# Optimization experiments

Hardware: AMD Instinct MI355X
Metric: run time of the kernel (lower is better)

Reference implementation:

```python
import jax, jax.numpy as jnp
import numpy as np

NODES = 81
NODE_DIM = 2
IN_DIM = NODES * NODE_DIM  # 162
D = 256
H = 16
HD = D // H
DFF = 2048
T, B, E = 1024, 8, 648


def _layernorm(x, w, b, eps=1e-5):
    m = x.mean(-1, keepdims=True)
    v = x.var(-1, keepdims=True)
    return (x - m) / jnp.sqrt(v + eps) * w + b


def setup_inputs() -> dict:
    key = jax.random.key(0)
    ks = jax.random.split(key, 12)
    s = 0.02
    W = lambda k, shape: jax.random.normal(k, shape, jnp.float32) * s
    return {
        "src": jax.random.normal(ks[0], (T, B, IN_DIM), jnp.float32),
        "edge_index": jax.random.randint(ks[1], (2, E), 0, NODES),
        "gcn_w": W(ks[2], (NODE_DIM, NODE_DIM)),
        "gcn_b": jnp.zeros((NODE_DIM,), jnp.float32),
        "fc_w": W(ks[3], (IN_DIM, D)),
        "fc_b": jnp.zeros((D,), jnp.float32),
        "wq": W(ks[4], (D, D)), "bq": jnp.zeros((D,), jnp.float32),
        "wk": W(ks[5], (D, D)), "bk": jnp.zeros((D,), jnp.float32),
        "wv": W(ks[6], (D, D)), "bv": jnp.zeros((D,), jnp.float32),
        "wo": W(ks[7], (D, D)), "bo": jnp.zeros((D,), jnp.float32),
        "ln1_w": jnp.ones((D,), jnp.float32), "ln1_b": jnp.zeros((D,), jnp.float32),
        "ffn_w1": W(ks[8], (D, DFF)), "ffn_b1": jnp.zeros((DFF,), jnp.float32),
        "ffn_w2": W(ks[9], (DFF, D)), "ffn_b2": jnp.zeros((D,), jnp.float32),
        "ln2_w": jnp.ones((D,), jnp.float32), "ln2_b": jnp.zeros((D,), jnp.float32),
        "dec_w": W(ks[10], (D, IN_DIM)), "dec_b": jnp.zeros((IN_DIM,), jnp.float32),
    }


def reference(src, edge_index, gcn_w, gcn_b, fc_w, fc_b, wq, bq, wk, bk, wv, bv,
              wo, bo, ln1_w, ln1_b, ffn_w1, ffn_b1, ffn_w2, ffn_b2, ln2_w, ln2_b,
              dec_w, dec_b):
    t, b, _ = src.shape
    # ---- batched GCNConv(2,2): all T*B tiny graphs share one adjacency ----
    # src[t,b] = [in_flow(81), out_flow(81)] -> node features [81, 2]
    xg = jnp.swapaxes(src.reshape(t, b, NODE_DIM, NODES), -1, -2)  # [T,B,81,2]
    row, col = edge_index[0], edge_index[1]
    A = jnp.zeros((NODES, NODES), src.dtype).at[col, row].add(1.0)
    A = A + jnp.eye(NODES, dtype=src.dtype)          # add self-loops
    deg = A.sum(1)
    dinv = jnp.where(deg > 0, 1.0 / jnp.sqrt(deg), 0.0)
    A_hat = dinv[:, None] * A * dinv[None, :]        # D^-1/2 (A+I) D^-1/2
    hg = jnp.einsum('ij,tbjc->tbic', A_hat, xg @ gcn_w) + gcn_b  # [T,B,81,2]
    # gcn_output.transpose(0,1).view(-1): channel-major flatten
    src2 = jnp.swapaxes(hg, -1, -2).reshape(t, b, IN_DIM)
    # ---- fc + positional encoding ----
    x = src2 @ fc_w + fc_b  # [T,B,D]
    pos = jnp.arange(t, dtype=jnp.float32)[:, None]
    div = jnp.exp(jnp.arange(0, D, 2, dtype=jnp.float32) * (-np.log(10000.0) / D))
    pe = jnp.zeros((t, D), x.dtype).at[:, 0::2].set(jnp.sin(pos * div))
    pe = pe.at[:, 1::2].set(jnp.cos(pos * div))
    x = x + pe[:, None, :]
    # ---- TransformerEncoderLayer (post-norm, relu, causal mask, eval) ----
    q = (x @ wq + bq).reshape(t, b, H, HD)
    k = (x @ wk + bk).reshape(t, b, H, HD)
    v = (x @ wv + bv).reshape(t, b, H, HD)
    scores = jnp.einsum('tbhd,sbhd->bhts', q, k) / jnp.sqrt(jnp.asarray(HD, x.dtype))
    causal = jnp.tril(jnp.ones((t, t), bool))
    scores = jnp.where(causal, scores, jnp.finfo(x.dtype).min)
    attn = jax.nn.softmax(scores, axis=-1)
    ctx = jnp.einsum('bhts,sbhd->tbhd', attn, v).reshape(t, b, D) @ wo + bo
    x = _layernorm(x + ctx, ln1_w, ln1_b)
    ff = jax.nn.relu(x @ ffn_w1 + ffn_b1) @ ffn_w2 + ffn_b2
    x = _layernorm(x + ff, ln2_w, ln2_b)
    return x @ dec_w + dec_b  # [T,B,162]
```

## Files before the change

kernel.cpp:

```cpp
#include <hip/hip_runtime.h>
#include <math.h>

#define T_    1024
#define B_    8
#define D_    256
#define H_    16
#define HD_   16
#define DFF_  2048
#define NODES_ 81
#define INDIM_ 162
#define E_    648
#define M_    (T_*B_)

typedef __bf16 bf16x8 __attribute__((ext_vector_type(8)));
typedef float  f32x4  __attribute__((ext_vector_type(4)));
typedef unsigned short ushort_t;
typedef unsigned int   uint_t;

union bfpack { bf16x8 v; uint_t u[4]; };

__device__ __forceinline__ ushort_t f2bf(float f) {
    union { float f; uint_t u; } c; c.f = f;
    uint_t u = c.u;
    uint_t r = u + 0x7fffu + ((u >> 16) & 1u);
    return (ushort_t)(r >> 16);
}

__device__ __forceinline__ uint_t fbits(float f) {
    union { float f; uint_t u; } c; c.f = f;
    return c.u;
}

__device__ __forceinline__ bf16x8 zero8() {
    bf16x8 v;
#pragma unroll
    for (int e = 0; e < 8; e++) v[e] = (__bf16)0.0f;
    return v;
}

__device__ __forceinline__ void gload_lds16(const void* g, void* l) {
    __builtin_amdgcn_global_load_lds(
        (const __attribute__((address_space(1))) void*)g,
        (__attribute__((address_space(3))) void*)l, 16, 0, 0);
}

__device__ __forceinline__ void trans_tile(
        const float* __restrict__ in, ushort_t* __restrict__ out,
        float (*tile)[33], int K, int N, int Kp, int bx, int by) {
    int k0 = bx * 32, n0 = by * 32;
    int tx = threadIdx.x & 31, ty = threadIdx.x >> 5;
#pragma unroll
    for (int i = 0; i < 4; i++) {
        int r = k0 + ty + i * 8, c = n0 + tx;
        tile[ty + i * 8][tx] = (r < K && c < N) ? in[(size_t)r * N + c] : 0.f;
    }
    __syncthreads();
#pragma unroll
    for (int i = 0; i < 4; i++) {
        int r = n0 + ty + i * 8, c = k0 + tx;
        out[(size_t)r * Kp + c] = f2bf(tile[tx][ty + i * 8]);
    }
}

__global__ __launch_bounds__(256) void prep_all(
        const int* __restrict__ edge, const float* __restrict__ gcn_w,
        const float* __restrict__ gcn_b, const float* __restrict__ fc_w,
        const float* __restrict__ fc_b, const float* __restrict__ src,
        const float* __restrict__ wq, const float* __restrict__ wk,
        const float* __restrict__ wv, const float* __restrict__ wo,
        const float* __restrict__ dec_w, const float* __restrict__ w1,
        const float* __restrict__ w2,
        const float* __restrict__ bq, const float* __restrict__ bk,
        const float* __restrict__ bv,
        ushort_t* __restrict__ weffT, float* __restrict__ beff,
        ushort_t* __restrict__ srcb,
        ushort_t* __restrict__ wqkvT, ushort_t* __restrict__ woT,
        ushort_t* __restrict__ dwT, ushort_t* __restrict__ w1T,
        ushort_t* __restrict__ w2T, float* __restrict__ qkvbias) {
    __shared__ float A[NODES_ * NODES_];
    __shared__ float dinv[NODES_];
    __shared__ float tile[32][33];
    int bid = blockIdx.x;
    int tid = threadIdx.x;
    if (bid < 82) {
        for (int i = tid; i < NODES_ * NODES_; i += 256) A[i] = 0.f;
        __syncthreads();
        for (int e = tid; e < E_; e += 256) {
            int r = edge[e];
            int c = edge[E_ + e];
            atomicAdd(&A[c * NODES_ + r], 1.0f);
        }
        __syncthreads();
        if (tid < NODES_) A[tid * NODES_ + tid] += 1.0f;
        __syncthreads();
        if (tid < NODES_) {
            float s = 0.f;
            for (int k = 0; k < NODES_; k++) s += A[tid * NODES_ + k];
            dinv[tid] = (s > 0.f) ? rsqrtf(s) : 0.f;
        }
        __syncthreads();
        int d = tid, j = bid;
        if (j < NODES_) {
            float s0 = 0.f, s1 = 0.f;
            for (int i = 0; i < NODES_; i++) {
                float a = dinv[i] * A[i * NODES_ + j] * dinv[j];
                s0 += a * fc_w[(0 * NODES_ + i) * D_ + d];
                s1 += a * fc_w[(1 * NODES_ + i) * D_ + d];
            }
            weffT[d * 192 + j]          = f2bf(gcn_w[0] * s0 + gcn_w[1] * s1);
            weffT[d * 192 + NODES_ + j] = f2bf(gcn_w[2] * s0 + gcn_w[3] * s1);
        } else {
            float t0 = 0.f, t1 = 0.f;
            for (int i = 0; i < NODES_; i++) {
                t0 += fc_w[(0 * NODES_ + i) * D_ + d];
                t1 += fc_w[(1 * NODES_ + i) * D_ + d];
            }
            beff[d] = fc_b[d] + gcn_b[0] * t0 + gcn_b[1] * t1;
            for (int c = INDIM_; c < 192; c++) weffT[d * 192 + c] = 0;
        }
    } else if (bid < 1426) {
        int l = bid - 82;
        if (l < 64)        trans_tile(wq,    wqkvT,          tile, D_,   D_,     D_,   l & 7,  l >> 3);
        else if (l < 128)  trans_tile(wk,    wqkvT + 65536,  tile, D_,   D_,     D_,   (l-64) & 7,  (l-64) >> 3);
        else if (l < 192)  trans_tile(wv,    wqkvT + 131072, tile, D_,   D_,     D_,   (l-128) & 7, (l-128) >> 3);
        else if (l < 256)  trans_tile(wo,    woT,            tile, D_,   D_,     D_,   (l-192) & 7, (l-192) >> 3);
        else if (l < 320)  trans_tile(dec_w, dwT,            tile, D_,   INDIM_, D_,   (l-256) & 7, (l-256) >> 3);
        else if (l < 832)  trans_tile(w1,    w1T,            tile, D_,   DFF_,   D_,   (l-320) & 7, (l-320) >> 3);
        else               trans_tile(w2,    w2T,            tile, DFF_, D_,     DFF_, (l-832) & 63, (l-832) >> 6);
    } else if (bid == 1426) {
#pragma unroll
        for (int k = 0; k < 3; k++) {
            int i = k * 256 + tid;
            qkvbias[i] = (i < 256) ? bq[i] : ((i < 512) ? bk[i - 256] : bv[i - 512]);
        }
    } else {
        int r = bid - 1427;
        if (tid < 192)
            srcb[(size_t)r * 192 + tid] =
                (tid < INDIM_) ? f2bf(src[(size_t)r * INDIM_ + tid]) : (ushort_t)0;
    }
}

enum { EP_PE = 0, EP_QKV = 1, EP_PLAIN = 2, EP_RELU = 3, EP_DEC = 4, EP_PART = 5 };

template <int EPI, int TM, int KS>
__global__ __launch_bounds__(256) void gemm_bf16(
        const ushort_t* __restrict__ A, const ushort_t* __restrict__ BT,
        const float* __restrict__ bias, float* __restrict__ Cf,
        ushort_t* __restrict__ Cb, int M, int N, int K) {
    __shared__ ushort_t sA[TM * 64];
    __shared__ ushort_t sB[128 * 64];
    int tid = threadIdx.x;
    int w = tid >> 6, lane = tid & 63;
    int cc = lane & 15, q = lane >> 4;
    int bm = blockIdx.y * TM, bn = blockIdx.x * 128;
    int part = (KS > 1) ? blockIdx.z : 0;
    int kbeg = part * (K / KS), kend = kbeg + K / KS;

    int srow = (lane >> 3);
    int sslot = lane & 7;

    const int NJ = (TM == 128) ? 4 : 2;
    int mbase = (TM == 128) ? ((w >> 1) * 64) : 0;
    int nbase = (TM == 128) ? ((w & 1) * 64) : (w * 32);

    f32x4 acc[4][NJ];
#pragma unroll
    for (int i = 0; i < 4; i++)
#pragma unroll
        for (int j = 0; j < NJ; j++)
#pragma unroll
            for (int e = 0; e < 4; e++) acc[i][j][e] = 0.f;

    for (int k0 = kbeg; k0 < kend; k0 += 64) {
        if (TM == 128) {
#pragma unroll
            for (int i = 0; i < 4; i++) {
                int r = w * 32 + i * 8 + srow;
                const ushort_t* ga = A + (size_t)(bm + r) * K + k0 + ((sslot ^ (r & 7)) * 8);
                gload_lds16(ga, &sA[(w * 32 + i * 8) * 64]);
            }
        } else {
#pragma unroll
            for (int i = 0; i < 2; i++) {
                int r = w * 16 + i * 8 + srow;
                const ushort_t* ga = A + (size_t)(bm + r) * K + k0 + ((sslot ^ (r & 7)) * 8);
                gload_lds16(ga, &sA[(w * 16 + i * 8) * 64]);
            }
        }
#pragma unroll
        for (int i = 0; i < 4; i++) {
            int r = w * 32 + i * 8 + srow;
            const ushort_t* gb = BT + (size_t)(bn + r) * K + k0 + ((sslot ^ (r & 7)) * 8);
            gload_lds16(gb, &sB[(w * 32 + i * 8) * 64]);
        }
        __syncthreads();
#pragma unroll
        for (int ks = 0; ks < 2; ks++) {
            bf16x8 af[4], bfr[NJ];
#pragma unroll
            for (int i = 0; i < 4; i++) {
                int m = mbase + i * 16 + cc;
                int off = m * 64 + (((ks * 4 + q) ^ (cc & 7)) * 8);
                af[i] = *(const bf16x8*)&sA[off];
            }
#pragma unroll
            for (int j = 0; j < NJ; j++) {
                int n = nbase + j * 16 + cc;
                int off = n * 64 + (((ks * 4 + q) ^ (cc & 7)) * 8);
                bfr[j] = *(const bf16x8*)&sB[off];
            }
#pragma unroll
            for (int i = 0; i < 4; i++)
#pragma unroll
                for (int j = 0; j < NJ; j++)
                    acc[i][j] = __builtin_amdgcn_mfma_f32_16x16x32_bf16(af[i], bfr[j], acc[i][j], 0, 0, 0);
        }
        __syncthreads();
    }

#pragma unroll
    for (int i = 0; i < 4; i++) {
#pragma unroll
        for (int j = 0; j < NJ; j++) {
            int col = bn + nbase + j * 16 + cc;
            float bv = 0.f;
            if (EPI == EP_DEC) bv = (col < INDIM_) ? bias[col] : 0.f;
            else if (EPI != EP_PART) bv = bias[col];
#pragma unroll
            for (int reg = 0; reg < 4; reg++) {
                int row = bm + mbase + i * 16 + q * 4 + reg;
                float v = acc[i][j][reg] + bv;
                if (EPI == EP_PE) {
                    int t = row >> 3;
                    float freq = __expf((float)(col & ~1) * (-9.210340371976184f / 256.f));
                    float ang = (float)t * freq;
                    v += (col & 1) ? __cosf(ang) : __sinf(ang);
                    Cf[(size_t)row * N + col] = v;
                    Cb[(size_t)row * N + col] = f2bf(v);
                } else if (EPI == EP_QKV) {
                    int t = row >> 3, b = row & 7;
                    int nn = col & 255, which = col >> 8;
                    int h = nn >> 4, hd = nn & 15;
                    float vq = (which == 0) ? v * 0.25f : v;
                    Cb[(size_t)which * 2097152 +
                       ((size_t)((b * H_ + h) * T_ + t)) * HD_ + hd] = f2bf(vq);
                } else if (EPI == EP_PLAIN) {
                    Cf[(size_t)row * N + col] = v;
                } else if (EPI == EP_RELU) {
                    v = fmaxf(v, 0.f);
                    Cb[(size_t)row * N + col] = f2bf(v);
                } else if (EPI == EP_DEC) {
                    if (col < INDIM_) Cf[(size_t)row * INDIM_ + col] = v;
                } else if (EPI == EP_PART) {
                    Cf[(size_t)part * M * N + (size_t)row * N + col] = v;
                }
            }
        }
    }
}

__global__ __launch_bounds__(256) void attn_mfma(
        const ushort_t* __restrict__ Qb, const ushort_t* __restrict__ Kb,
        const ushort_t* __restrict__ Vb, float* __restrict__ partO,
        float* __restrict__ partL) {
    const int qc_of[20] = {0,1,2,2,3,3,4,4,4,5,5,5,6,6,6,6,7,7,7,7};
    const int kp_of[20] = {0,0,0,1,0,1,0,1,2,0,1,2,0,1,2,3,0,1,2,3};
    int slot = blockIdx.x;
    int qc = qc_of[slot], kp = kp_of[slot];
    int bh = blockIdx.y;
    int tid = threadIdx.x;
    int w = tid >> 6, lane = tid & 63;
    int cc = lane & 15, q = lane >> 4;
    int qb0 = qc * 128;
    int kbeg = kp * 4;
    int kend = 2 * (qc + 1);
    if (kend > kbeg + 4) kend = kbeg + 4;

    __shared__ ushort_t VTs[2][16 * 72];

    const ushort_t* Qp = Qb + (size_t)bh * (T_ * HD_);
    const ushort_t* Kp = Kb + (size_t)bh * (T_ * HD_);
    const ushort_t* Vp = Vb + (size_t)bh * (T_ * HD_);

    bf16x8 qf[2];
#pragma unroll
    for (int i = 0; i < 2; i++) {
        if (q < 2)
            qf[i] = *(const bf16x8*)&Qp[(size_t)(qb0 + w * 32 + i * 16 + cc) * HD_ + q * 8];
        else
            qf[i] = zero8();
    }

    bf16x8 ones8;
#pragma unroll
    for (int e = 0; e < 8; e++) ones8[e] = (__bf16)1.0f;

    f32x4 ot[2], ls[2];
#pragma unroll
    for (int i = 0; i < 2; i++)
#pragma unroll
        for (int e = 0; e < 4; e++) { ot[i][e] = 0.f; ls[i][e] = 0.f; }

    int qmaxw = qb0 + w * 32 + 31;

    for (int kb = kbeg; kb < kend; kb++) {
        ushort_t* vbuf = VTs[kb & 1];
        {
            int r = tid >> 2, c0 = (tid & 3) * 4;
            ushort4 vv = *(const ushort4*)&Vp[(size_t)(kb * 64 + r) * HD_ + c0];
            vbuf[(c0 + 0) * 72 + r] = vv.x;
            vbuf[(c0 + 1) * 72 + r] = vv.y;
            vbuf[(c0 + 2) * 72 + r] = vv.z;
            vbuf[(c0 + 3) * 72 + r] = vv.w;
        }
        __syncthreads();
        if (kb * 64 > qmaxw) continue;

        bf16x8 kf[4];
#pragma unroll
        for (int j = 0; j < 4; j++) {
            if (q < 2)
                kf[j] = *(const bf16x8*)&Kp[(size_t)(kb * 64 + j * 16 + cc) * HD_ + q * 8];
            else
                kf[j] = zero8();
        }

        f32x4 s[2][4];
#pragma unroll
        for (int j = 0; j < 4; j++)
#pragma unroll
            for (int i = 0; i < 2; i++) {
                f32x4 z;
#pragma unroll
                for (int e = 0; e < 4; e++) z[e] = 0.f;
                s[i][j] = __builtin_amdgcn_mfma_f32_16x16x32_bf16(kf[j], qf[i], z, 0, 0, 0);
            }

#pragma unroll
        for (int j = 0; j < 4; j++) {
            bfpack af;
            const uint_t* vt = (const uint_t*)&vbuf[cc * 72 + j * 16 + q * 4];
            af.u[0] = vt[0]; af.u[1] = vt[1]; af.u[2] = 0u; af.u[3] = 0u;
            int key0 = kb * 64 + j * 16 + q * 4;
#pragma unroll
            for (int i = 0; i < 2; i++) {
                float p0 = __expf(s[i][j][0]);
                float p1 = __expf(s[i][j][1]);
                float p2 = __expf(s[i][j][2]);
                float p3 = __expf(s[i][j][3]);
                if (kb * 64 + j * 16 + 15 > qb0 + w * 32 + i * 16) {
                    int qrow = qb0 + w * 32 + i * 16 + cc;
                    if (key0 + 0 > qrow) p0 = 0.f;
                    if (key0 + 1 > qrow) p1 = 0.f;
                    if (key0 + 2 > qrow) p2 = 0.f;
                    if (key0 + 3 > qrow) p3 = 0.f;
                }
                bfpack pf;
                pf.u[0] = (fbits(p0) >> 16) | (fbits(p1) & 0xffff0000u);
                pf.u[1] = (fbits(p2) >> 16) | (fbits(p3) & 0xffff0000u);
                pf.u[2] = 0u; pf.u[3] = 0u;
                ot[i] = __builtin_amdgcn_mfma_f32_16x16x32_bf16(af.v, pf.v, ot[i], 0, 0, 0);
                ls[i] = __builtin_amdgcn_mfma_f32_16x16x32_bf16(ones8, pf.v, ls[i], 0, 0, 0);
            }
        }
    }

    int base = (bh * 20 + slot) * 128;
#pragma unroll
    for (int i = 0; i < 2; i++) {
        int row = w * 32 + i * 16 + cc;
        *(f32x4*)&partO[((size_t)(base + row)) * 16 + q * 4] = ot[i];
        if (q == 0) partL[base + row] = ls[i][0];
    }
}

__global__ __launch_bounds__(256) void attn_reduce(
        const float* __restrict__ partO, const float* __restrict__ partL,
        ushort_t* __restrict__ ctxb) {
    const int cum[9] = {0, 1, 2, 4, 6, 9, 12, 16, 20};
    int qc = blockIdx.x, bh = blockIdx.y;
    int row = threadIdx.x >> 1, dh = threadIdx.x & 1;
    int p0 = cum[qc], p1 = cum[qc + 1];
    float o[8];
#pragma unroll
    for (int e = 0; e < 8; e++) o[e] = 0.f;
    float l = 0.f;
    for (int p = p0; p < p1; p++) {
        size_t base = ((size_t)bh * 20 + p) * 128 + row;
        const float4 a = *(const float4*)&partO[base * 16 + dh * 8];
        const float4 b4 = *(const float4*)&partO[base * 16 + dh * 8 + 4];
        o[0] += a.x; o[1] += a.y; o[2] += a.z; o[3] += a.w;
        o[4] += b4.x; o[5] += b4.y; o[6] += b4.z; o[7] += b4.w;
        l += partL[base];
    }
    float inv = 1.f / l;
    int t = qc * 128 + row, b = bh >> 4, h = bh & 15;
    ushort_t* op = ctxb + ((size_t)t * B_ + b) * D_ + h * HD_ + dh * 8;
    ushort4 u0, u1;
    u0.x = f2bf(o[0] * inv); u0.y = f2bf(o[1] * inv);
    u0.z = f2bf(o[2] * inv); u0.w = f2bf(o[3] * inv);
    u1.x = f2bf(o[4] * inv); u1.y = f2bf(o[5] * inv);
    u1.z = f2bf(o[6] * inv); u1.w = f2bf(o[7] * inv);
    *(ushort4*)&op[0] = u0;
    *(ushort4*)&op[4] = u1;
}

template <int NP, bool HASB>
__global__ __launch_bounds__(256) void ln_kernel(
        const float* __restrict__ X, const float* __restrict__ P0,
        const float* __restrict__ P1, const float* __restrict__ RB,
        const float* __restrict__ w, const float* __restrict__ b,
        float* __restrict__ out, ushort_t* __restrict__ outb) {
    int wv = threadIdx.x >> 6, lane = threadIdx.x & 63;
    int row = blockIdx.x * 4 + wv;
    int c = lane * 4;
    const float4 x4 = *(const float4*)&X[(size_t)row * D_ + c];
    const float4 p4 = *(const float4*)&P0[(size_t)row * D_ + c];
    float v0 = x4.x + p4.x, v1 = x4.y + p4.y, v2 = x4.z + p4.z, v3 = x4.w + p4.w;
    if (NP == 2) {
        const float4 q4 = *(const float4*)&P1[(size_t)row * D_ + c];
        v0 += q4.x; v1 += q4.y; v2 += q4.z; v3 += q4.w;
    }
    if (HASB) {
        const float4 r4 = *(const float4*)&RB[c];
        v0 += r4.x; v1 += r4.y; v2 += r4.z; v3 += r4.w;
    }
    float s  = v0 + v1 + v2 + v3;
    float sq = v0 * v0 + v1 * v1 + v2 * v2 + v3 * v3;
    for (int off = 32; off; off >>= 1) {
        s  += __shfl_xor(s, off);
        sq += __shfl_xor(sq, off);
    }
    float mean = s * (1.f / 256.f);
    float var  = sq * (1.f / 256.f) - mean * mean;
    float rstd = rsqrtf(var + 1e-5f);
    float o0 = (v0 - mean) * rstd * w[c + 0] + b[c + 0];
    float o1 = (v1 - mean) * rstd * w[c + 1] + b[c + 1];
    float o2 = (v2 - mean) * rstd * w[c + 2] + b[c + 2];
    float o3 = (v3 - mean) * rstd * w[c + 3] + b[c + 3];
    float4 o; o.x = o0; o.y = o1; o.z = o2; o.w = o3;
    *(float4*)&out[(size_t)row * D_ + c] = o;
    ushort4 ob;
    ob.x = f2bf(o0); ob.y = f2bf(o1); ob.z = f2bf(o2); ob.w = f2bf(o3);
    *(ushort4*)&outb[(size_t)row * D_ + c] = ob;
}

extern "C" void kernel_launch(void* const* d_in, const int* in_sizes, int n_in,
                              void* d_out, int out_size, void* d_ws, size_t ws_size,
                              hipStream_t stream) {
    (void)in_sizes; (void)n_in; (void)out_size; (void)ws_size;
    const float* src     = (const float*)d_in[0];
    const int*   edge    = (const int*)d_in[1];
    const float* gcn_w   = (const float*)d_in[2];
    const float* gcn_b   = (const float*)d_in[3];
    const float* fc_w    = (const float*)d_in[4];
    const float* fc_b    = (const float*)d_in[5];
    const float* wq      = (const float*)d_in[6];
    const float* bq      = (const float*)d_in[7];
    const float* wk      = (const float*)d_in[8];
    const float* bk      = (const float*)d_in[9];
    const float* wv      = (const float*)d_in[10];
    const float* bv      = (const float*)d_in[11];
    const float* wo      = (const float*)d_in[12];
    const float* bo      = (const float*)d_in[13];
    const float* ln1_w   = (const float*)d_in[14];
    const float* ln1_b   = (const float*)d_in[15];
    const float* ffn_w1  = (const float*)d_in[16];
    const float* ffn_b1  = (const float*)d_in[17];
    const float* ffn_w2  = (const float*)d_in[18];
    const float* ffn_b2  = (const float*)d_in[19];
    const float* ln2_w   = (const float*)d_in[20];
    const float* ln2_b   = (const float*)d_in[21];
    const float* dec_w   = (const float*)d_in[22];
    const float* dec_b   = (const float*)d_in[23];
    float* out = (float*)d_out;

    float* ws = (float*)d_ws;
    float* beff    = ws;
    float* qkvbias = ws + 256;
    float* x0      = ws + 1024;
    float* tmp     = x0  + 2097152;
    float* tmp2    = tmp + 2097152;
    float* x1      = tmp2 + 2097152;
    float* x2s     = x1  + 2097152;
    ushort_t* ub   = (ushort_t*)(ws + 10486784);
    ushort_t* srcb = ub;
    ushort_t* x0b  = ub + 1572864;
    ushort_t* x1b  = x0b + 2097152;
    ushort_t* x2b  = x1b + 2097152;
    ushort_t* ctxb = x2b + 2097152;
    ushort_t* hb   = ctxb + 2097152;
    ushort_t* qkvb = hb + 16777216;
    ushort_t* weffT= qkvb + 6291456;
    ushort_t* wqkvT= weffT + 49152;
    ushort_t* woT  = wqkvT + 196608;
    ushort_t* w1T  = woT + 65536;
    ushort_t* w2T  = w1T + 524288;
    ushort_t* dwT  = w2T + 524288;
    float* partO = (float*)hb;
    float* partL = partO + 5242880;

    prep_all<<<9619, 256, 0, stream>>>(edge, gcn_w, gcn_b, fc_w, fc_b, src,
                                       wq, wk, wv, wo, dec_w, ffn_w1, ffn_w2,
                                       bq, bk, bv, weffT, beff, srcb,
                                       wqkvT, woT, dwT, w1T, w2T, qkvbias);

    gemm_bf16<EP_PE, 64, 1><<<dim3(2, 128), 256, 0, stream>>>(srcb, weffT, beff, x0, x0b, M_, D_, 192);
    gemm_bf16<EP_QKV, 64, 1><<<dim3(6, 128), 256, 0, stream>>>(x0b, wqkvT, qkvbias, nullptr, qkvb, M_, 768, D_);
    attn_mfma<<<dim3(20, 128), 256, 0, stream>>>(qkvb, qkvb + 2097152, qkvb + 4194304, partO, partL);
    attn_reduce<<<dim3(8, 128), 256, 0, stream>>>(partO, partL, ctxb);
    gemm_bf16<EP_PLAIN, 64, 1><<<dim3(2, 128), 256, 0, stream>>>(ctxb, woT, bo, tmp, nullptr, M_, D_, D_);
    ln_kernel<1, false><<<2048, 256, 0, stream>>>(x0, tmp, nullptr, nullptr, ln1_w, ln1_b, x1, x1b);
    gemm_bf16<EP_RELU, 128, 1><<<dim3(16, 64), 256, 0, stream>>>(x1b, w1T, ffn_b1, nullptr, hb, M_, DFF_, D_);
    gemm_bf16<EP_PART, 64, 2><<<dim3(2, 128, 2), 256, 0, stream>>>(hb, w2T, nullptr, tmp, nullptr, M_, D_, DFF_);
    ln_kernel<2, true><<<2048, 256, 0, stream>>>(x1, tmp, tmp2, ffn_b2, ln2_w, ln2_b, x2s, x2b);
    gemm_bf16<EP_DEC, 64, 1><<<dim3(2, 128), 256, 0, stream>>>(x2b, dwT, dec_b, out, nullptr, M_, D_, D_);
}
```

Measured before the change: 234.8 us.

## Store V transposed from QKV GEMM, drop attention LDS staging, split Wo GEMM

The QKV GEMM epilogue now writes V in a head-dim-major (transposed) layout, so the attention kernel can load V fragments straight from global memory. This removes the shared-memory transpose and the per-iteration __syncthreads, and the masked-out tail of the key loop now breaks instead of continuing. The output-projection GEMM is split along K into two partial outputs that the LN1 kernel sums, which doubles the block count. The final LN also skips its unused fp32 output write. The costs are strided global V stores in the GEMM epilogue and extra partial-buffer traffic.

```diff
diff --git a/kernel.cpp b/kernel.cpp
--- a/kernel.cpp
+++ b/kernel.cpp
@@ -242,9 +242,15 @@
                     int t = row >> 3, b = row & 7;
                     int nn = col & 255, which = col >> 8;
                     int h = nn >> 4, hd = nn & 15;
-                    float vq = (which == 0) ? v * 0.25f : v;
-                    Cb[(size_t)which * 2097152 +
-                       ((size_t)((b * H_ + h) * T_ + t)) * HD_ + hd] = f2bf(vq);
+                    if (which == 0) {
+                        Cb[((size_t)((b * H_ + h) * T_ + t)) * HD_ + hd] = f2bf(v * 0.25f);
+                    } else if (which == 1) {
+                        Cb[(size_t)2097152 +
+                           ((size_t)((b * H_ + h) * T_ + t)) * HD_ + hd] = f2bf(v);
+                    } else {
+                        Cb[(size_t)4194304 +
+                           ((size_t)((b * H_ + h) * HD_ + hd)) * T_ + t] = f2bf(v);
+                    }
                 } else if (EPI == EP_PLAIN) {
                     Cf[(size_t)row * N + col] = v;
                 } else if (EPI == EP_RELU) {
@@ -262,7 +268,7 @@
 
 __global__ __launch_bounds__(256) void attn_mfma(
         const ushort_t* __restrict__ Qb, const ushort_t* __restrict__ Kb,
-        const ushort_t* __restrict__ Vb, float* __restrict__ partO,
+        const ushort_t* __restrict__ VTb, float* __restrict__ partO,
         float* __restrict__ partL) {
     const int qc_of[20] = {0,1,2,2,3,3,4,4,4,5,5,5,6,6,6,6,7,7,7,7};
     const int kp_of[20] = {0,0,0,1,0,1,0,1,2,0,1,2,0,1,2,3,0,1,2,3};
@@ -277,11 +283,9 @@
     int kend = 2 * (qc + 1);
     if (kend > kbeg + 4) kend = kbeg + 4;
 
-    __shared__ ushort_t VTs[2][16 * 72];
-
-    const ushort_t* Qp = Qb + (size_t)bh * (T_ * HD_);
-    const ushort_t* Kp = Kb + (size_t)bh * (T_ * HD_);
-    const ushort_t* Vp = Vb + (size_t)bh * (T_ * HD_);
+    const ushort_t* Qp  = Qb  + (size_t)bh * (T_ * HD_);
+    const ushort_t* Kp  = Kb  + (size_t)bh * (T_ * HD_);
+    const ushort_t* VTp = VTb + (size_t)bh * (HD_ * T_) + (size_t)cc * T_;
 
     bf16x8 qf[2];
 #pragma unroll
@@ -305,25 +309,17 @@
     int qmaxw = qb0 + w * 32 + 31;
 
     for (int kb = kbeg; kb < kend; kb++) {
-        ushort_t* vbuf = VTs[kb & 1];
-        {
-            int r = tid >> 2, c0 = (tid & 3) * 4;
-            ushort4 vv = *(const ushort4*)&Vp[(size_t)(kb * 64 + r) * HD_ + c0];
-            vbuf[(c0 + 0) * 72 + r] = vv.x;
-            vbuf[(c0 + 1) * 72 + r] = vv.y;
-            vbuf[(c0 + 2) * 72 + r] = vv.z;
-            vbuf[(c0 + 3) * 72 + r] = vv.w;
-        }
-        __syncthreads();
-        if (kb * 64 > qmaxw) continue;
+        if (kb * 64 > qmaxw) break;
 
         bf16x8 kf[4];
+        uint2 vv[4];
 #pragma unroll
         for (int j = 0; j < 4; j++) {
             if (q < 2)
                 kf[j] = *(const bf16x8*)&Kp[(size_t)(kb * 64 + j * 16 + cc) * HD_ + q * 8];
             else
                 kf[j] = zero8();
+            vv[j] = *(const uint2*)&VTp[kb * 64 + j * 16 + q * 4];
         }
 
         f32x4 s[2][4];
@@ -340,8 +336,7 @@
 #pragma unroll
         for (int j = 0; j < 4; j++) {
             bfpack af;
-            const uint_t* vt = (const uint_t*)&vbuf[cc * 72 + j * 16 + q * 4];
-            af.u[0] = vt[0]; af.u[1] = vt[1]; af.u[2] = 0u; af.u[3] = 0u;
+            af.u[0] = vv[j].x; af.u[1] = vv[j].y; af.u[2] = 0u; af.u[3] = 0u;
             int key0 = kb * 64 + j * 16 + q * 4;
 #pragma unroll
             for (int i = 0; i < 2; i++) {
@@ -406,7 +401,7 @@
     *(ushort4*)&op[4] = u1;
 }
 
-template <int NP, bool HASB>
+template <int NP, bool HASB, bool WF>
 __global__ __launch_bounds__(256) void ln_kernel(
         const float* __restrict__ X, const float* __restrict__ P0,
         const float* __restrict__ P1, const float* __restrict__ RB,
@@ -439,8 +434,10 @@
     float o1 = (v1 - mean) * rstd * w[c + 1] + b[c + 1];
     float o2 = (v2 - mean) * rstd * w[c + 2] + b[c + 2];
     float o3 = (v3 - mean) * rstd * w[c + 3] + b[c + 3];
-    float4 o; o.x = o0; o.y = o1; o.z = o2; o.w = o3;
-    *(float4*)&out[(size_t)row * D_ + c] = o;
+    if (WF) {
+        float4 o; o.x = o0; o.y = o1; o.z = o2; o.w = o3;
+        *(float4*)&out[(size_t)row * D_ + c] = o;
+    }
     ushort4 ob;
     ob.x = f2bf(o0); ob.y = f2bf(o1); ob.z = f2bf(o2); ob.w = f2bf(o3);
     *(ushort4*)&outb[(size_t)row * D_ + c] = ob;
@@ -510,10 +507,10 @@
     gemm_bf16<EP_QKV, 64, 1><<<dim3(6, 128), 256, 0, stream>>>(x0b, wqkvT, qkvbias, nullptr, qkvb, M_, 768, D_);
     attn_mfma<<<dim3(20, 128), 256, 0, stream>>>(qkvb, qkvb + 2097152, qkvb + 4194304, partO, partL);
     attn_reduce<<<dim3(8, 128), 256, 0, stream>>>(partO, partL, ctxb);
-    gemm_bf16<EP_PLAIN, 64, 1><<<dim3(2, 128), 256, 0, stream>>>(ctxb, woT, bo, tmp, nullptr, M_, D_, D_);
-    ln_kernel<1, false><<<2048, 256, 0, stream>>>(x0, tmp, nullptr, nullptr, ln1_w, ln1_b, x1, x1b);
+    gemm_bf16<EP_PART, 64, 2><<<dim3(2, 128, 2), 256, 0, stream>>>(ctxb, woT, nullptr, tmp, nullptr, M_, D_, D_);
+    ln_kernel<2, true, true><<<2048, 256, 0, stream>>>(x0, tmp, tmp2, bo, ln1_w, ln1_b, x1, x1b);
     gemm_bf16<EP_RELU, 128, 1><<<dim3(16, 64), 256, 0, stream>>>(x1b, w1T, ffn_b1, nullptr, hb, M_, DFF_, D_);
     gemm_bf16<EP_PART, 64, 2><<<dim3(2, 128, 2), 256, 0, stream>>>(hb, w2T, nullptr, tmp, nullptr, M_, D_, DFF_);
-    ln_kernel<2, true><<<2048, 256, 0, stream>>>(x1, tmp, tmp2, ffn_b2, ln2_w, ln2_b, x2s, x2b);
+    ln_kernel<2, true, false><<<2048, 256, 0, stream>>>(x1, tmp, tmp2, ffn_b2, ln2_w, ln2_b, x2s, x2b);
     gemm_bf16<EP_DEC, 64, 1><<<dim3(2, 128), 256, 0, stream>>>(x2b, dwT, dec_b, out, nullptr, M_, D_, D_);
 }
```

Result: slower. 244.1 us (+4.0%).
